# Kernel optimization log

Hardware: AMD Instinct MI355X
Metric: run time of the kernel (lower is better)

Reference implementation:

```python
import jax, jax.numpy as jnp
import numpy as np

N = 50000   # nodes
E = 500000  # edges
H = 128     # hidden_dim


def setup_inputs() -> dict:
    key = jax.random.key(0)
    ks = jax.random.split(key, 8)
    w = lambda k, shp: jax.random.normal(k, shp, jnp.float32) * 0.02
    return {
        "edge_idx": jax.random.randint(ks[0], (E, 2), 0, N, dtype=jnp.int32),
        "node_feats": jax.random.normal(ks[1], (N, H), jnp.float32),
        "edge_feats": jax.random.normal(ks[2], (E, H), jnp.float32),
        # edge MLP params: Linear(3H,H) -> ReLU -> Linear(H,H) -> LayerNorm(H)
        "We1": w(ks[3], (3 * H, H)), "be1": jnp.zeros((H,), jnp.float32),
        "We2": w(ks[4], (H, H)),     "be2": jnp.zeros((H,), jnp.float32),
        "ge": jnp.ones((H,), jnp.float32), "bge": jnp.zeros((H,), jnp.float32),
        # node MLP params: Linear(2H,H) -> ReLU -> Linear(H,H) -> LayerNorm(H)
        "Wn1": w(ks[5], (2 * H, H)), "bn1": jnp.zeros((H,), jnp.float32),
        "Wn2": w(ks[6], (H, H)),     "bn2": jnp.zeros((H,), jnp.float32),
        "gn": jnp.ones((H,), jnp.float32), "bgn": jnp.zeros((H,), jnp.float32),
    }


def layer_norm(x, g, b, eps=1e-5):
    m = jnp.mean(x, axis=-1, keepdims=True)
    v = jnp.var(x, axis=-1, keepdims=True)
    return (x - m) * jax.lax.rsqrt(v + eps) * g + b


def reference(edge_idx, node_feats, edge_feats,
              We1, be1, We2, be2, ge, bge,
              Wn1, bn1, Wn2, bn2, gn, bgn):
    senders = edge_idx[:, 0]
    receivers = edge_idx[:, 1]
    # edge update: gather endpoints, concat with edge feats, MLP + LN
    e_in = jnp.concatenate([node_feats[senders], node_feats[receivers], edge_feats], axis=-1)  # [E, 3H]
    edge_update = layer_norm(jax.nn.relu(e_in @ We1 + be1) @ We2 + be2, ge, bge)               # [E, H]
    # faithful to source: scatter-add of edge_feats (NOT edge_update) into receivers
    acc = jax.ops.segment_sum(edge_feats, receivers, num_segments=node_feats.shape[0])          # [N, H]
    n_in = jnp.concatenate([node_feats, acc], axis=-1)                                          # [N, 2H]
    node_update = layer_norm(jax.nn.relu(n_in @ Wn1 + bn1) @ Wn2 + bn2, gn, bgn)                # [N, H]
    return node_feats + node_update, edge_feats + edge_update
```

## Files before the change

kernel.cpp:

```cpp
#include <hip/hip_runtime.h>
#include <hip/hip_bf16.h>

#define DI __device__ __forceinline__

typedef __attribute__((ext_vector_type(8))) short short8;
typedef __attribute__((ext_vector_type(4))) short short4v;
typedef __attribute__((ext_vector_type(4))) float floatx4;

constexpr int NN = 50000;
constexpr int NE = 500000;
constexpr int H  = 128;
constexpr int NB1 = (NN + 255) / 256;

constexpr size_t OFF_BF   = 262144;
constexpr size_t OFF_PS   = 327680;
constexpr size_t OFF_PR   = 13127680;
constexpr size_t OFF_CNT  = 25927680;
constexpr size_t OFF_TMP  = 26127680;
constexpr size_t OFF_RS   = 26327680;
constexpr size_t OFF_CUR  = 26527680;
constexpr size_t OFF_BSUM = 26727680;
constexpr size_t OFF_CSR  = 26728704;

constexpr int WF_TOTAL = 131072;
constexpr int BIASF_FLOATS = 8*2048;
constexpr int PREP_TOTAL = WF_TOTAL + BIASF_FLOATS + NN;

DI short f2bf(float f){ __bf16 b = (__bf16)f; return __builtin_bit_cast(short, b); }
DI float bf2f(short s){ return __builtin_bit_cast(float, ((unsigned)(unsigned short)s) << 16); }

__global__ __launch_bounds__(256) void prep_kernel(
    const float* __restrict__ We1, const float* __restrict__ We2,
    const float* __restrict__ Wn1, const float* __restrict__ Wn2,
    const float* __restrict__ be1, const float* __restrict__ be2,
    const float* __restrict__ ge,  const float* __restrict__ bge,
    const float* __restrict__ bn1, const float* __restrict__ bn2,
    const float* __restrict__ gn,  const float* __restrict__ bgn,
    short* __restrict__ wf, float* __restrict__ bf, int* __restrict__ cnt)
{
  int t = blockIdx.x*256 + threadIdx.x;
  if (t < WF_TOTAL) {
    int blk = t >> 14, u = t & 16383;
    int j = u & 7, l = (u>>3)&63, nt = (u>>9)&7, ks = u>>12;
    const float* src; int roff; bool blayout = false;
    switch (blk) {
      case 0: src = We1; roff = 0;   break;
      case 1: src = We1; roff = 128; break;
      case 2: src = We1; roff = 256; break;
      case 3: src = We2; roff = 0;   break;
      case 4: src = Wn1; roff = 0;   break;
      case 5: src = Wn1; roff = 128; break;
      case 6: src = Wn2; roff = 0;   break;
      default: src = We2; roff = 0; blayout = true; break;
    }
    int row = blayout ? (32*ks + 16*(j>>2) + 4*(l>>4) + (j&3))
                      : (roff + 32*ks + 8*(l>>4) + j);
    int col = 16*nt + (l&15);
    wf[t] = f2bf(src[row*H + col]);
  } else if (t < WF_TOTAL + BIASF_FLOATS) {
    int tb = t - WF_TOTAL;
    int arr = tb >> 11, u = tb & 2047;
    int r = u&3, l = (u>>2)&63, mt = u>>8;
    int feat = 16*mt + 4*(l>>4) + r;
    const float* s;
    switch (arr) {
      case 0: s = be1; break; case 1: s = be2; break;
      case 2: s = ge;  break; case 3: s = bge; break;
      case 4: s = bn1; break; case 5: s = bn2; break;
      case 6: s = gn;  break; default: s = bgn; break;
    }
    bf[tb] = s[feat];
  } else if (t < PREP_TOTAL) {
    cnt[t - WF_TOTAL - BIASF_FLOATS] = 0;
  }
}

__global__ __launch_bounds__(256) void hist_kernel(const int* __restrict__ ei, int* __restrict__ cnt){
  int e = blockIdx.x*256 + threadIdx.x;
  if (e < NE) atomicAdd(&cnt[ei[2*e+1]], 1);
}

__global__ __launch_bounds__(256) void scan1_kernel(const int* __restrict__ cnt,
                                                    int* __restrict__ tmp, int* __restrict__ blocksum){
  __shared__ int s[256];
  int t = threadIdx.x, i = blockIdx.x*256 + t;
  int v = (i < NN) ? cnt[i] : 0;
  s[t] = v; __syncthreads();
#pragma unroll
  for (int o=1; o<256; o<<=1){
    int u = (t >= o) ? s[t-o] : 0;
    __syncthreads();
    s[t] += u;
    __syncthreads();
  }
  if (i < NN) tmp[i] = s[t];
  if (t == 255) blocksum[blockIdx.x] = s[255];
}

__global__ __launch_bounds__(256) void scan3_kernel(const int* __restrict__ cnt, const int* __restrict__ tmp,
                                                    const int* __restrict__ blocksum,
                                                    int* __restrict__ rowstart, int* __restrict__ cursor){
  __shared__ int pfx;
  int t = threadIdx.x, bid = blockIdx.x;
  if (t < 64){
    int p = 0;
    for (int k = t; k < bid; k += 64) p += blocksum[k];
#pragma unroll
    for (int o=32; o>0; o>>=1) p += __shfl_down(p, o);
    if (t == 0) pfx = p;
  }
  __syncthreads();
  int i = bid*256 + t;
  if (i < NN){
    int rs = tmp[i] - cnt[i] + pfx;
    rowstart[i] = rs; cursor[i] = rs;
  }
}

__global__ __launch_bounds__(256) void scatter_kernel(const int* __restrict__ ei,
                                                      int* __restrict__ cursor, int* __restrict__ csr){
  int e = blockIdx.x*256 + threadIdx.x;
  if (e < NE){
    int r = ei[2*e+1];
    int p = atomicAdd(&cursor[r], 1);
    csr[p] = e;
  }
}

__global__ __launch_bounds__(256) void segsum_kernel(const int* __restrict__ csr,
                                                     const int* __restrict__ rowstart,
                                                     const int* __restrict__ cnt,
                                                     const float* __restrict__ edge_feats,
                                                     float* __restrict__ acc){
  int tid = threadIdx.x;
  int w = tid>>6, l = tid&63;
  int hh = l>>5, q = l&31;
  int n = blockIdx.x*8 + w*2 + hh;
  if (n >= NN) return;
  int start = rowstart[n], deg = cnt[n];
  floatx4 s0 = floatx4{0.f,0.f,0.f,0.f};
  floatx4 s1 = floatx4{0.f,0.f,0.f,0.f};
  int k = 0;
  for (; k+8 <= deg; k += 8){
    int e0 = csr[start+k],   e1 = csr[start+k+1];
    int e2 = csr[start+k+2], e3 = csr[start+k+3];
    int e4 = csr[start+k+4], e5 = csr[start+k+5];
    int e6 = csr[start+k+6], e7 = csr[start+k+7];
    floatx4 v0 = *(const floatx4*)(edge_feats + (size_t)e0*H + 4*q);
    floatx4 v1 = *(const floatx4*)(edge_feats + (size_t)e1*H + 4*q);
    floatx4 v2 = *(const floatx4*)(edge_feats + (size_t)e2*H + 4*q);
    floatx4 v3 = *(const floatx4*)(edge_feats + (size_t)e3*H + 4*q);
    floatx4 v4 = *(const floatx4*)(edge_feats + (size_t)e4*H + 4*q);
    floatx4 v5 = *(const floatx4*)(edge_feats + (size_t)e5*H + 4*q);
    floatx4 v6 = *(const floatx4*)(edge_feats + (size_t)e6*H + 4*q);
    floatx4 v7 = *(const floatx4*)(edge_feats + (size_t)e7*H + 4*q);
    s0 += v0; s1 += v1; s0 += v2; s1 += v3;
    s0 += v4; s1 += v5; s0 += v6; s1 += v7;
  }
  for (; k+4 <= deg; k += 4){
    int e0 = csr[start+k],   e1 = csr[start+k+1];
    int e2 = csr[start+k+2], e3 = csr[start+k+3];
    floatx4 v0 = *(const floatx4*)(edge_feats + (size_t)e0*H + 4*q);
    floatx4 v1 = *(const floatx4*)(edge_feats + (size_t)e1*H + 4*q);
    floatx4 v2 = *(const floatx4*)(edge_feats + (size_t)e2*H + 4*q);
    floatx4 v3 = *(const floatx4*)(edge_feats + (size_t)e3*H + 4*q);
    s0 += v0; s1 += v1; s0 += v2; s1 += v3;
  }
  for (; k < deg; ++k){
    int e = csr[start+k];
    s0 += *(const floatx4*)(edge_feats + (size_t)e*H + 4*q);
  }
  s0 += s1;
  *(floatx4*)(acc + (size_t)n*H + 4*q) = s0;
}

__global__ __launch_bounds__(256) void pproj_kernel(
    const float* __restrict__ node_feats,
    const short* __restrict__ wsf, const short* __restrict__ wrf,
    const float* __restrict__ b1f,
    short* __restrict__ Ps, short* __restrict__ Pr)
{
  const int tid = threadIdx.x;
  const int w = tid>>6, l = tid&63, g = l>>4, lo = l&15;
  int row = blockIdx.x*64 + w*16 + lo;
  bool valid = row < NN;
  int rowc = valid ? row : (NN-1);
  const float* sp = node_feats + (size_t)rowc*H;

  short8 ein[4];
#pragma unroll
  for (int ks=0; ks<4; ++ks){
    const int koff = ks*32 + g*8;
    floatx4 f0 = *(const floatx4*)(sp + koff);
    floatx4 f1 = *(const floatx4*)(sp + koff + 4);
    ein[ks][0]=f2bf(f0[0]); ein[ks][1]=f2bf(f0[1]); ein[ks][2]=f2bf(f0[2]); ein[ks][3]=f2bf(f0[3]);
    ein[ks][4]=f2bf(f1[0]); ein[ks][5]=f2bf(f1[1]); ein[ks][6]=f2bf(f1[2]); ein[ks][7]=f2bf(f1[3]);
  }

  floatx4 as[8], ar[8];
#pragma unroll
  for (int mt=0; mt<8; ++mt){ as[mt] = floatx4{0,0,0,0}; ar[mt] = floatx4{0,0,0,0}; }
#pragma unroll
  for (int ks=0; ks<4; ++ks){
#pragma unroll
    for (int mt=0; mt<8; ++mt){
      short8 wv = *(const short8*)(wsf + ((ks*8+mt)*64 + l)*8);
      as[mt] = __builtin_amdgcn_mfma_f32_16x16x32_bf16(wv, ein[ks], as[mt], 0,0,0);
      short8 wv2 = *(const short8*)(wrf + ((ks*8+mt)*64 + l)*8);
      ar[mt] = __builtin_amdgcn_mfma_f32_16x16x32_bf16(wv2, ein[ks], ar[mt], 0,0,0);
    }
  }

  if (valid){
    short* ps = Ps + (size_t)rowc*H + g*32;
    short* pr = Pr + (size_t)rowc*H + g*32;
#pragma unroll
    for (int mt=0; mt<8; ++mt){
      floatx4 bv = *(const floatx4*)(b1f + (mt*64+l)*4);
      short4v vs, vr;
#pragma unroll
      for (int r=0; r<4; ++r){ vs[r] = f2bf(as[mt][r] + bv[r]); vr[r] = f2bf(ar[mt][r]); }
      *(short4v*)(ps + mt*4) = vs;
      *(short4v*)(pr + mt*4) = vr;
    }
  }
}

template<int R>
__global__ __launch_bounds__(512) void edge_kernel(
    const int* __restrict__ edge_idx,
    const float* __restrict__ edge_feats,
    const short* __restrict__ Ps, const short* __restrict__ Pr,
    const short* __restrict__ wef, const short* __restrict__ w2fB,
    const float* __restrict__ b2f,
    const float* __restrict__ gf,  const float* __restrict__ bgf,
    float* __restrict__ out_edge)
{
  extern __shared__ short smem[];
  short* wA = smem;
  short* wB = smem + 16384;
  const int tid = threadIdx.x;
  const int w = tid>>6, l = tid&63, g = l>>4, lo = l&15;

  int rowc[R]; bool valid[R]; int2 se[R];
#pragma unroll
  for (int b=0; b<R; ++b){
    int row = blockIdx.x*(8*16*R) + w*(16*R) + b*16 + lo;
    valid[b] = row < NE;
    rowc[b]  = valid[b] ? row : (NE-1);
    se[b] = *(const int2*)(edge_idx + 2*rowc[b]);
  }

#pragma unroll
  for (int rnd=0; rnd<4; ++rnd){
    int o = (rnd*512 + tid)*8;
    *(short8*)(wA + o) = *(const short8*)(wef  + o);
    *(short8*)(wB + o) = *(const short8*)(w2fB + o);
  }

  short8 vs[4], vr[4];
  {
    const short* ps = Ps + (size_t)se[0].x*H + g*32;
    const short* pr = Pr + (size_t)se[0].y*H + g*32;
#pragma unroll
    for (int m2=0; m2<4; ++m2){
      vs[m2] = *(const short8*)(ps + m2*8);
      vr[m2] = *(const short8*)(pr + m2*8);
    }
  }
  floatx4 ef[8];
  {
    const float* sp = edge_feats + (size_t)rowc[0]*H;
#pragma unroll
    for (int ks=0; ks<4; ++ks){
      ef[2*ks]   = *(const floatx4*)(sp + ks*32 + g*8);
      ef[2*ks+1] = *(const floatx4*)(sp + ks*32 + g*8 + 4);
    }
  }
  __syncthreads();

#pragma unroll
  for (int b=0; b<R; ++b){
    short8 ein[4];
#pragma unroll
    for (int ks=0; ks<4; ++ks){
      ein[ks][0]=f2bf(ef[2*ks][0]);   ein[ks][1]=f2bf(ef[2*ks][1]);
      ein[ks][2]=f2bf(ef[2*ks][2]);   ein[ks][3]=f2bf(ef[2*ks][3]);
      ein[ks][4]=f2bf(ef[2*ks+1][0]); ein[ks][5]=f2bf(ef[2*ks+1][1]);
      ein[ks][6]=f2bf(ef[2*ks+1][2]); ein[ks][7]=f2bf(ef[2*ks+1][3]);
    }

    if (b+1 < R){
      const float* sp = edge_feats + (size_t)rowc[b+1]*H;
#pragma unroll
      for (int ks=0; ks<4; ++ks){
        ef[2*ks]   = *(const floatx4*)(sp + ks*32 + g*8);
        ef[2*ks+1] = *(const floatx4*)(sp + ks*32 + g*8 + 4);
      }
    }

    floatx4 acc[8];
#pragma unroll
    for (int mt=0; mt<8; ++mt) acc[mt] = floatx4{0.f,0.f,0.f,0.f};
#pragma unroll
    for (int ks=0; ks<4; ++ks){
#pragma unroll
      for (int mt=0; mt<8; ++mt){
        short8 wv = *(const short8*)(wA + ((ks*8+mt)*64 + l)*8);
        acc[mt] = __builtin_amdgcn_mfma_f32_16x16x32_bf16(wv, ein[ks], acc[mt], 0,0,0);
      }
    }

#pragma unroll
    for (int m2=0; m2<4; ++m2)
#pragma unroll
      for (int r=0; r<4; ++r){
        acc[2*m2][r]   += bf2f(vs[m2][r])   + bf2f(vr[m2][r]);
        acc[2*m2+1][r] += bf2f(vs[m2][4+r]) + bf2f(vr[m2][4+r]);
      }

    if (b+1 < R){
      const short* ps = Ps + (size_t)se[b+1].x*H + g*32;
      const short* pr = Pr + (size_t)se[b+1].y*H + g*32;
#pragma unroll
      for (int m2=0; m2<4; ++m2){
        vs[m2] = *(const short8*)(ps + m2*8);
        vr[m2] = *(const short8*)(pr + m2*8);
      }
    }

    short8 hb[4];
#pragma unroll
    for (int s=0; s<4; ++s){
#pragma unroll
      for (int r=0; r<4; ++r){
        float v0 = acc[2*s][r];
        float v1 = acc[2*s+1][r];
        hb[s][r]   = f2bf(v0 > 0.f ? v0 : 0.f);
        hb[s][4+r] = f2bf(v1 > 0.f ? v1 : 0.f);
      }
    }

#pragma unroll
    for (int mt=0; mt<8; ++mt) acc[mt] = *(const floatx4*)(b2f + (mt*64+l)*4);
#pragma unroll
    for (int s=0; s<4; ++s){
#pragma unroll
      for (int mt=0; mt<8; ++mt){
        short8 wv = *(const short8*)(wB + ((s*8+mt)*64 + l)*8);
        acc[mt] = __builtin_amdgcn_mfma_f32_16x16x32_bf16(wv, hb[s], acc[mt], 0,0,0);
      }
    }

    float sum = 0.f, ssq = 0.f;
#pragma unroll
    for (int mt=0; mt<8; ++mt)
#pragma unroll
      for (int r=0; r<4; ++r){ float v = acc[mt][r]; sum += v; ssq += v*v; }
    sum += __shfl_xor(sum, 16); ssq += __shfl_xor(ssq, 16);
    sum += __shfl_xor(sum, 32); ssq += __shfl_xor(ssq, 32);
    const float mean = sum * (1.f/H);
    const float var  = ssq * (1.f/H) - mean*mean;
    const float rs   = rsqrtf(var + 1e-5f);

    const float* resid = edge_feats + (size_t)rowc[b]*H;
    float* outp = out_edge + (size_t)rowc[b]*H;
#pragma unroll
    for (int mt=0; mt<8; ++mt){
      floatx4 gv  = *(const floatx4*)(gf  + (mt*64+l)*4);
      floatx4 bgv = *(const floatx4*)(bgf + (mt*64+l)*4);
      floatx4 efr = *(const floatx4*)(resid + mt*16 + g*4);
      floatx4 o;
#pragma unroll
      for (int r=0; r<4; ++r) o[r] = efr[r] + (acc[mt][r]-mean)*rs*gv[r] + bgv[r];
      if (valid[b]) *(floatx4*)(outp + mt*16 + g*4) = o;
    }
  }
}

__global__ __launch_bounds__(256) void node_kernel(
    const float* __restrict__ node_feats,
    const short* __restrict__ w1f, const short* __restrict__ w2f,
    const float* __restrict__ b1f, const float* __restrict__ b2f,
    const float* __restrict__ gf,  const float* __restrict__ bgf,
    float* __restrict__ out_node)
{
  __shared__ short lds_h[4*2048];
  const int tid = threadIdx.x;
  const int w = tid>>6, l = tid&63, g = l>>4, lo = l&15;
  short* ldsw = lds_h + w*2048;

  int row = blockIdx.x*64 + w*16 + lo;
  bool valid = row < NN;
  int rowc = valid ? row : (NN-1);
  const float* sp0 = node_feats + (size_t)rowc*H;
  const float* sp1 = out_node   + (size_t)rowc*H;

  floatx4 acc1[8];
#pragma unroll
  for (int mt=0; mt<8; ++mt) acc1[mt] = *(const floatx4*)(b1f + (mt*64+l)*4);

#pragma unroll
  for (int ks=0; ks<8; ++ks){
    const float* sp = (ks<4) ? sp0 : sp1;
    const int koff = (ks&3)*32 + g*8;
    floatx4 f0 = *(const floatx4*)(sp + koff);
    floatx4 f1 = *(const floatx4*)(sp + koff + 4);
    short8 ein;
    ein[0]=f2bf(f0[0]); ein[1]=f2bf(f0[1]); ein[2]=f2bf(f0[2]); ein[3]=f2bf(f0[3]);
    ein[4]=f2bf(f1[0]); ein[5]=f2bf(f1[1]); ein[6]=f2bf(f1[2]); ein[7]=f2bf(f1[3]);
#pragma unroll
    for (int mt=0; mt<8; ++mt){
      short8 wv = *(const short8*)(w1f + ((ks*8+mt)*64 + l)*8);
      acc1[mt] = __builtin_amdgcn_mfma_f32_16x16x32_bf16(wv, ein, acc1[mt], 0,0,0);
    }
  }

#pragma unroll
  for (int mt=0; mt<8; ++mt){
    short4v hv;
#pragma unroll
    for (int r=0; r<4; ++r){
      float v = acc1[mt][r];
      hv[r] = f2bf(v > 0.f ? v : 0.f);
    }
    int off = (lo*256 + mt*32 + g*8) ^ ((lo&7)<<4);
    *(short4v*)((char*)ldsw + off) = hv;
  }

  floatx4 acc2[8];
#pragma unroll
  for (int mt=0; mt<8; ++mt) acc2[mt] = *(const floatx4*)(b2f + (mt*64+l)*4);

#pragma unroll
  for (int s=0; s<4; ++s){
    int roff = (lo*256 + s*64 + g*16) ^ ((lo&7)<<4);
    short8 hb = *(const short8*)((char*)ldsw + roff);
#pragma unroll
    for (int mt=0; mt<8; ++mt){
      short8 wv = *(const short8*)(w2f + ((s*8+mt)*64 + l)*8);
      acc2[mt] = __builtin_amdgcn_mfma_f32_16x16x32_bf16(wv, hb, acc2[mt], 0,0,0);
    }
  }

  float sum = 0.f, ssq = 0.f;
#pragma unroll
  for (int mt=0; mt<8; ++mt)
#pragma unroll
    for (int r=0; r<4; ++r){ float v = acc2[mt][r]; sum += v; ssq += v*v; }
  sum += __shfl_xor(sum, 16); ssq += __shfl_xor(ssq, 16);
  sum += __shfl_xor(sum, 32); ssq += __shfl_xor(ssq, 32);
  const float mean = sum * (1.f/H);
  const float var  = ssq * (1.f/H) - mean*mean;
  const float rs   = rsqrtf(var + 1e-5f);

#pragma unroll
  for (int mt=0; mt<8; ++mt){
    floatx4 gv  = *(const floatx4*)(gf  + (mt*64+l)*4);
    floatx4 bgv = *(const floatx4*)(bgf + (mt*64+l)*4);
    floatx4 nf  = *(const floatx4*)(node_feats + (size_t)rowc*H + mt*16 + g*4);
    floatx4 o;
#pragma unroll
    for (int r=0; r<4; ++r) o[r] = nf[r] + (acc2[mt][r]-mean)*rs*gv[r] + bgv[r];
    if (valid) *(floatx4*)(out_node + (size_t)rowc*H + mt*16 + g*4) = o;
  }
}

extern "C" void kernel_launch(void* const* d_in, const int* in_sizes, int n_in,
                              void* d_out, int out_size, void* d_ws, size_t ws_size,
                              hipStream_t stream)
{
  const int*   edge_idx   = (const int*)  d_in[0];
  const float* node_feats = (const float*)d_in[1];
  const float* edge_feats = (const float*)d_in[2];
  const float* We1=(const float*)d_in[3];  const float* be1=(const float*)d_in[4];
  const float* We2=(const float*)d_in[5];  const float* be2=(const float*)d_in[6];
  const float* ge =(const float*)d_in[7];  const float* bge=(const float*)d_in[8];
  const float* Wn1=(const float*)d_in[9];  const float* bn1=(const float*)d_in[10];
  const float* Wn2=(const float*)d_in[11]; const float* bn2=(const float*)d_in[12];
  const float* gn =(const float*)d_in[13]; const float* bgn=(const float*)d_in[14];

  float* out_node = (float*)d_out;
  float* out_edge = out_node + (size_t)NN*H;

  char* ws = (char*)d_ws;
  short* wf      = (short*)ws;
  float* bf      = (float*)(ws + OFF_BF);
  short* Ps      = (short*)(ws + OFF_PS);
  short* Pr      = (short*)(ws + OFF_PR);
  int* cnt       = (int*)(ws + OFF_CNT);
  int* tmp       = (int*)(ws + OFF_TMP);
  int* rowstart  = (int*)(ws + OFF_RS);
  int* cursor    = (int*)(ws + OFF_CUR);
  int* blocksum  = (int*)(ws + OFF_BSUM);
  int* csr       = (int*)(ws + OFF_CSR);

  short* wsf  = wf;
  short* wrf  = wf + 16384;
  short* wef  = wf + 32768;
  short* wn1f = wf + 65536;
  short* wn2f = wf + 98304;
  short* w2fB = wf + 114688;
  float* b1f  = bf;         float* b2f  = bf + 2048;
  float* gef  = bf + 4096;  float* bgef = bf + 6144;
  float* bn1f = bf + 8192;  float* bn2f = bf + 10240;
  float* gnf  = bf + 12288; float* bgnf = bf + 14336;

  prep_kernel<<<(PREP_TOTAL + 255)/256, 256, 0, stream>>>(
      We1, We2, Wn1, Wn2, be1, be2, ge, bge, bn1, bn2, gn, bgn, wf, bf, cnt);

  hist_kernel<<<(NE+255)/256, 256, 0, stream>>>(edge_idx, cnt);
  scan1_kernel<<<NB1, 256, 0, stream>>>(cnt, tmp, blocksum);
  scan3_kernel<<<NB1, 256, 0, stream>>>(cnt, tmp, blocksum, rowstart, cursor);
  scatter_kernel<<<(NE+255)/256, 256, 0, stream>>>(edge_idx, cursor, csr);

  pproj_kernel<<<(NN+63)/64, 256, 0, stream>>>(node_feats, wsf, wrf, b1f, Ps, Pr);

  edge_kernel<2><<<(NE + 255)/256, 512, 65536, stream>>>(
      edge_idx, edge_feats, Ps, Pr, wef, w2fB, b2f, gef, bgef, out_edge);

  segsum_kernel<<<(NN+7)/8, 256, 0, stream>>>(csr, rowstart, cnt, edge_feats, out_node);

  node_kernel<<<(NN+63)/64, 256, 0, stream>>>(
      node_feats, wn1f, wn2f, bn1f, bn2f, gnf, bgnf, out_node);
}
```

Measured before the change: 351.9 us.

## Fuse segment-sum into edge kernel via interleaved heterogeneous block roles

Merges the segment-sum gather kernel and the edge MLP kernel into one launch, where block index mod 5 decides whether a block runs the compute-heavy edge MLP (2 of 5) or the memory-bound segment sum (3 of 5). The aim is to overlap the bandwidth-bound gather with the MFMA-bound edge work and drop one kernel launch and its tail. In exchange, the segsum blocks now run at 512 threads with a 64KB dynamic shared memory allocation they never use, which can limit occupancy. Each segsum block also now covers 16 nodes instead of 8.

```diff
diff --git a/kernel.cpp b/kernel.cpp
--- a/kernel.cpp
+++ b/kernel.cpp
@@ -25,6 +25,11 @@
 constexpr int WF_TOTAL = 131072;
 constexpr int BIASF_FLOATS = 8*2048;
 constexpr int PREP_TOTAL = WF_TOTAL + BIASF_FLOATS + NN;
+
+constexpr int EB = (NE + 255) / 256;
+constexpr int SB = (NN + 15) / 16;
+constexpr int FUSE_GROUPS = (SB + 2) / 3 > (EB + 1) / 2 ? (SB + 2) / 3 : (EB + 1) / 2;
+constexpr int FUSE_GRID = FUSE_GROUPS * 5;
 
 DI short f2bf(float f){ __bf16 b = (__bf16)f; return __builtin_bit_cast(short, b); }
 DI float bf2f(short s){ return __builtin_bit_cast(float, ((unsigned)(unsigned short)s) << 16); }
@@ -127,53 +132,6 @@
   }
 }
 
-__global__ __launch_bounds__(256) void segsum_kernel(const int* __restrict__ csr,
-                                                     const int* __restrict__ rowstart,
-                                                     const int* __restrict__ cnt,
-                                                     const float* __restrict__ edge_feats,
-                                                     float* __restrict__ acc){
-  int tid = threadIdx.x;
-  int w = tid>>6, l = tid&63;
-  int hh = l>>5, q = l&31;
-  int n = blockIdx.x*8 + w*2 + hh;
-  if (n >= NN) return;
-  int start = rowstart[n], deg = cnt[n];
-  floatx4 s0 = floatx4{0.f,0.f,0.f,0.f};
-  floatx4 s1 = floatx4{0.f,0.f,0.f,0.f};
-  int k = 0;
-  for (; k+8 <= deg; k += 8){
-    int e0 = csr[start+k],   e1 = csr[start+k+1];
-    int e2 = csr[start+k+2], e3 = csr[start+k+3];
-    int e4 = csr[start+k+4], e5 = csr[start+k+5];
-    int e6 = csr[start+k+6], e7 = csr[start+k+7];
-    floatx4 v0 = *(const floatx4*)(edge_feats + (size_t)e0*H + 4*q);
-    floatx4 v1 = *(const floatx4*)(edge_feats + (size_t)e1*H + 4*q);
-    floatx4 v2 = *(const floatx4*)(edge_feats + (size_t)e2*H + 4*q);
-    floatx4 v3 = *(const floatx4*)(edge_feats + (size_t)e3*H + 4*q);
-    floatx4 v4 = *(const floatx4*)(edge_feats + (size_t)e4*H + 4*q);
-    floatx4 v5 = *(const floatx4*)(edge_feats + (size_t)e5*H + 4*q);
-    floatx4 v6 = *(const floatx4*)(edge_feats + (size_t)e6*H + 4*q);
-    floatx4 v7 = *(const floatx4*)(edge_feats + (size_t)e7*H + 4*q);
-    s0 += v0; s1 += v1; s0 += v2; s1 += v3;
-    s0 += v4; s1 += v5; s0 += v6; s1 += v7;
-  }
-  for (; k+4 <= deg; k += 4){
-    int e0 = csr[start+k],   e1 = csr[start+k+1];
-    int e2 = csr[start+k+2], e3 = csr[start+k+3];
-    floatx4 v0 = *(const floatx4*)(edge_feats + (size_t)e0*H + 4*q);
-    floatx4 v1 = *(const floatx4*)(edge_feats + (size_t)e1*H + 4*q);
-    floatx4 v2 = *(const floatx4*)(edge_feats + (size_t)e2*H + 4*q);
-    floatx4 v3 = *(const floatx4*)(edge_feats + (size_t)e3*H + 4*q);
-    s0 += v0; s1 += v1; s0 += v2; s1 += v3;
-  }
-  for (; k < deg; ++k){
-    int e = csr[start+k];
-    s0 += *(const floatx4*)(edge_feats + (size_t)e*H + 4*q);
-  }
-  s0 += s1;
-  *(floatx4*)(acc + (size_t)n*H + 4*q) = s0;
-}
-
 __global__ __launch_bounds__(256) void pproj_kernel(
     const float* __restrict__ node_feats,
     const short* __restrict__ wsf, const short* __restrict__ wrf,
@@ -227,25 +185,77 @@
 }
 
 template<int R>
-__global__ __launch_bounds__(512) void edge_kernel(
+__global__ __launch_bounds__(512) void fused_kernel(
     const int* __restrict__ edge_idx,
     const float* __restrict__ edge_feats,
     const short* __restrict__ Ps, const short* __restrict__ Pr,
     const short* __restrict__ wef, const short* __restrict__ w2fB,
     const float* __restrict__ b2f,
     const float* __restrict__ gf,  const float* __restrict__ bgf,
-    float* __restrict__ out_edge)
+    float* __restrict__ out_edge,
+    const int* __restrict__ csr, const int* __restrict__ rowstart,
+    const int* __restrict__ cnt, float* __restrict__ acc_out)
 {
   extern __shared__ short smem[];
+  const int bid = blockIdx.x;
+  const int tid = threadIdx.x;
+  const int m5 = bid % 5, gq = bid / 5;
+
+  if (m5 >= 2) {
+    int sb = gq*3 + (m5 - 2);
+    if (sb >= SB) return;
+    int w = tid>>6, l = tid&63;
+    int hh = l>>5, q = l&31;
+    int n = sb*16 + w*2 + hh;
+    if (n >= NN) return;
+    int start = rowstart[n], deg = cnt[n];
+    floatx4 s0 = floatx4{0.f,0.f,0.f,0.f};
+    floatx4 s1 = floatx4{0.f,0.f,0.f,0.f};
+    int k = 0;
+    for (; k+8 <= deg; k += 8){
+      int e0 = csr[start+k],   e1 = csr[start+k+1];
+      int e2 = csr[start+k+2], e3 = csr[start+k+3];
+      int e4 = csr[start+k+4], e5 = csr[start+k+5];
+      int e6 = csr[start+k+6], e7 = csr[start+k+7];
+      floatx4 v0 = *(const floatx4*)(edge_feats + (size_t)e0*H + 4*q);
+      floatx4 v1 = *(const floatx4*)(edge_feats + (size_t)e1*H + 4*q);
+      floatx4 v2 = *(const floatx4*)(edge_feats + (size_t)e2*H + 4*q);
+      floatx4 v3 = *(const floatx4*)(edge_feats + (size_t)e3*H + 4*q);
+      floatx4 v4 = *(const floatx4*)(edge_feats + (size_t)e4*H + 4*q);
+      floatx4 v5 = *(const floatx4*)(edge_feats + (size_t)e5*H + 4*q);
+      floatx4 v6 = *(const floatx4*)(edge_feats + (size_t)e6*H + 4*q);
+      floatx4 v7 = *(const floatx4*)(edge_feats + (size_t)e7*H + 4*q);
+      s0 += v0; s1 += v1; s0 += v2; s1 += v3;
+      s0 += v4; s1 += v5; s0 += v6; s1 += v7;
+    }
+    for (; k+4 <= deg; k += 4){
+      int e0 = csr[start+k],   e1 = csr[start+k+1];
+      int e2 = csr[start+k+2], e3 = csr[start+k+3];
+      floatx4 v0 = *(const floatx4*)(edge_feats + (size_t)e0*H + 4*q);
+      floatx4 v1 = *(const floatx4*)(edge_feats + (size_t)e1*H + 4*q);
+      floatx4 v2 = *(const floatx4*)(edge_feats + (size_t)e2*H + 4*q);
+      floatx4 v3 = *(const floatx4*)(edge_feats + (size_t)e3*H + 4*q);
+      s0 += v0; s1 += v1; s0 += v2; s1 += v3;
+    }
+    for (; k < deg; ++k){
+      int e = csr[start+k];
+      s0 += *(const floatx4*)(edge_feats + (size_t)e*H + 4*q);
+    }
+    s0 += s1;
+    *(floatx4*)(acc_out + (size_t)n*H + 4*q) = s0;
+    return;
+  }
+
+  int eb = gq*2 + m5;
+  if (eb >= EB) return;
   short* wA = smem;
   short* wB = smem + 16384;
-  const int tid = threadIdx.x;
   const int w = tid>>6, l = tid&63, g = l>>4, lo = l&15;
 
   int rowc[R]; bool valid[R]; int2 se[R];
 #pragma unroll
   for (int b=0; b<R; ++b){
-    int row = blockIdx.x*(8*16*R) + w*(16*R) + b*16 + lo;
+    int row = eb*(8*16*R) + w*(16*R) + b*16 + lo;
     valid[b] = row < NE;
     rowc[b]  = valid[b] ? row : (NE-1);
     se[b] = *(const int2*)(edge_idx + 2*rowc[b]);
@@ -516,10 +526,9 @@
 
   pproj_kernel<<<(NN+63)/64, 256, 0, stream>>>(node_feats, wsf, wrf, b1f, Ps, Pr);
 
-  edge_kernel<2><<<(NE + 255)/256, 512, 65536, stream>>>(
-      edge_idx, edge_feats, Ps, Pr, wef, w2fB, b2f, gef, bgef, out_edge);
-
-  segsum_kernel<<<(NN+7)/8, 256, 0, stream>>>(csr, rowstart, cnt, edge_feats, out_node);
+  fused_kernel<2><<<FUSE_GRID, 512, 65536, stream>>>(
+      edge_idx, edge_feats, Ps, Pr, wef, w2fB, b2f, gef, bgef, out_edge,
+      csr, rowstart, cnt, out_node);
 
   node_kernel<<<(NN+63)/64, 256, 0, stream>>>(
       node_feats, wn1f, wn2f, bn1f, bn2f, gnf, bgnf, out_node);
```

After: 371.7 us. 5.6% more time.
